# Kernel tuning notes

Measured on AMD Instinct MI355X. Metric: run time of the kernel, lower is better.

## Reference

```python
import jax, jax.numpy as jnp
import numpy as np

B, E, D, M = 128, 8, 512, 4
H = M * D


def setup_inputs() -> dict:
    key = jax.random.key(0)
    k = jax.random.split(key, 6)
    scale1 = 1.0 / np.sqrt(D)
    scale2 = 1.0 / np.sqrt(H)
    return {
        "features": jax.random.normal(k[0], (B, E, D), jnp.float32),
        "target_features": jax.random.normal(k[1], (B, E, D), jnp.float32),
        # batched params for the E x E grid of 2-layer MLPs
        "W1": jax.random.uniform(k[2], (E, E, D, H), jnp.float32, -scale1, scale1),
        "b1": jax.random.uniform(k[3], (E, E, H), jnp.float32, -scale1, scale1),
        "W2": jax.random.uniform(k[4], (E, E, H, D), jnp.float32, -scale2, scale2),
        "b2": jax.random.uniform(k[5], (E, E, D), jnp.float32, -scale2, scale2),
    }


def reference(features, target_features, W1, b1, W2, b2):
    # adapter (a, e) is applied to features[:, a]; all E^2 MLPs batched as grouped GEMMs
    # h: [B, A=E(adapted), E(inner), H]
    h = jax.nn.gelu(jnp.einsum('bad,aedh->baeh', features, W1) + b1, approximate=False)
    out = jnp.einsum('baeh,aehd->baed', h, W2) + b2  # [B, A, E, D]
    # per-(a,e) MSE against target_features[:, a], summed over grid, / num_experts
    err = out - target_features[:, :, None, :]
    per_pair_mse = jnp.mean(err * err, axis=(0, 3))  # [A, E]
    return jnp.sum(per_pair_mse) / E
```

## Files before the change

### kernel.cpp

```cpp
#include <hip/hip_runtime.h>
#include <math.h>


typedef float floatx4 __attribute__((ext_vector_type(4)));
typedef float floatx2 __attribute__((ext_vector_type(2)));
typedef __bf16 bf16x8 __attribute__((ext_vector_type(8)));
typedef unsigned short ushortx8 __attribute__((ext_vector_type(8)));

__device__ __forceinline__ unsigned short f2bf(float f) {
    unsigned u = __builtin_bit_cast(unsigned, f);
    u += 0x7fffu + ((u >> 16) & 1u);
    return (unsigned short)(u >> 16);
}

__device__ __forceinline__ void barrier_nd() {
    asm volatile("s_waitcnt lgkmcnt(0)" ::: "memory");
    __builtin_amdgcn_s_barrier();
}

#define LDSTR 40

__global__ __launch_bounds__(256, 3) void k_gemm1(
    const float* __restrict__ feat, const float* __restrict__ W1,
    const float* __restrict__ b1, unsigned short* __restrict__ hbuf)
{
    __shared__ __align__(16) unsigned short lB[2][128 * LDSTR];

    const int bi = blockIdx.x;
    const int xcd = bi & 7, slot = bi >> 3;
    const int pair = xcd * 8 + (slot >> 4);
    const int nt   = slot & 15;
    const int a    = pair >> 3;
    const int t = threadIdx.x;
    const int w = t >> 6, l = t & 63;
    const int lr = l & 15, lq = l >> 4;
    const int n_base = nt * 128;
    const int m0 = (w & 1) * 64;
    const int n0 = (w >> 1) * 64;

    const float* Bp = W1 + (size_t)pair * 512 * 2048 + n_base + 2 * l;
    const int bk0 = w * 8;
    const float* Af = feat + ((size_t)(m0 + lr) * 8 + a) * 512 + lq * 8;

    floatx2 bpf0[8], bpf1[8];

#define G1_LOADB(KT, S)                                                        \
    {                                                                          \
        _Pragma("unroll")                                                      \
        for (int jj = 0; jj < 8; ++jj)                                         \
            S[jj] = __builtin_nontemporal_load(                                \
                (const floatx2*)(Bp + (size_t)((KT) * 32 + bk0 + jj) * 2048)); \
    }

#define G1_STAGEB(S, BUF)                                                      \
    {                                                                          \
        ushortx8 v0, v1;                                                       \
        _Pragma("unroll")                                                      \
        for (int jj = 0; jj < 8; ++jj) {                                       \
            v0[jj] = f2bf(S[jj][0]);                                           \
            v1[jj] = f2bf(S[jj][1]);                                           \
        }                                                                      \
        *(ushortx8*)&lB[BUF][(2 * l) * LDSTR + bk0] = v0;                      \
        *(ushortx8*)&lB[BUF][(2 * l + 1) * LDSTR + bk0] = v1;                  \
    }

    floatx4 acc[4][4];
    const floatx4 zero = {0.f, 0.f, 0.f, 0.f};
    #pragma unroll
    for (int i = 0; i < 4; ++i)
        #pragma unroll
        for (int j = 0; j < 4; ++j) acc[i][j] = zero;

    G1_LOADB(0, bpf0)
    G1_LOADB(1, bpf1)
    G1_STAGEB(bpf0, 0)
    barrier_nd();

#define G1_BODY(KT, BUF, SLD, SST, GLD, GST)                                   \
    {                                                                          \
        bf16x8 bv[4];                                                          \
        _Pragma("unroll")                                                      \
        for (int j = 0; j < 4; ++j)                                            \
            bv[j] = __builtin_bit_cast(bf16x8,                                 \
                *(const ushortx8*)&lB[BUF][(n0 + 16 * j + lr) * LDSTR + lq * 8]); \
        floatx4 a0[4], a1[4];                                                  \
        _Pragma("unroll")                                                      \
        for (int i = 0; i < 4; ++i) {                                          \
            const float* p = Af + (size_t)(65536 * i) + (KT) * 32;             \
            a0[i] = *(const floatx4*)p;                                        \
            a1[i] = *(const floatx4*)(p + 4);                                  \
        }                                                                      \
        if (GLD) G1_LOADB((KT) + 2, SLD)                                       \
        bf16x8 af[4];                                                          \
        _Pragma("unroll")                                                      \
        for (int i = 0; i < 4; ++i) {                                          \
            ushortx8 v;                                                        \
            _Pragma("unroll")                                                  \
            for (int r = 0; r < 4; ++r) {                                      \
                v[r] = f2bf(a0[i][r]);                                         \
                v[4 + r] = f2bf(a1[i][r]);                                     \
            }                                                                  \
            af[i] = __builtin_bit_cast(bf16x8, v);                             \
        }                                                                      \
        __builtin_amdgcn_s_setprio(1);                                         \
        _Pragma("unroll")                                                      \
        for (int i = 0; i < 4; ++i)                                            \
            _Pragma("unroll")                                                  \
            for (int j = 0; j < 4; ++j)                                        \
                acc[i][j] = __builtin_amdgcn_mfma_f32_16x16x32_bf16(           \
                    af[i], bv[j], acc[i][j], 0, 0, 0);                         \
        __builtin_amdgcn_s_setprio(0);                                         \
        if (GST) G1_STAGEB(SST, (BUF) ^ 1)                                     \
        barrier_nd();                                                          \
    }

    #pragma unroll 1
    for (int kt = 0; kt < 16; kt += 2) {
        G1_BODY(kt,     0, bpf0, bpf1, (kt + 2 < 16), 1)
        G1_BODY(kt + 1, 1, bpf1, bpf0, (kt + 3 < 16), (kt + 2 < 16))
    }

    #pragma unroll
    for (int j = 0; j < 4; ++j) {
        const int col = n_base + n0 + 16 * j + lr;
        const float bias = b1[pair * 2048 + col];
        const size_t cbase = ((size_t)pair * 64 + (col >> 5)) * 128;
        const int cw = col & 31;
        #pragma unroll
        for (int i = 0; i < 4; ++i)
            #pragma unroll
            for (int r = 0; r < 4; ++r) {
                const int row = m0 + 16 * i + lq * 4 + r;
                float x = acc[i][j][r] + bias;
                float g = 0.5f * x * (1.0f + erff(x * 0.70710678118654752f));
                hbuf[(cbase + row) * 32 + cw] = f2bf(g);
            }
    }
#undef G1_LOADB
#undef G1_STAGEB
#undef G1_BODY
}

__global__ __launch_bounds__(256, 2) void k_gemm2(
    const unsigned short* __restrict__ hbuf, const float* __restrict__ W2,
    const float* __restrict__ b2, const float* __restrict__ tgt,
    float* __restrict__ partials)
{
    __shared__ __align__(16) unsigned short lB[2][64 * LDSTR];
    __shared__ float red[4];

    const int bi = blockIdx.x;
    const int xcd = bi & 7, slot = bi >> 3;
    const int pair = xcd * 8 + (slot >> 3);
    const int nt   = slot & 7;
    const int a    = pair >> 3;
    const int t = threadIdx.x;
    const int w = t >> 6, l = t & 63;
    const int lr = l & 15, lq = l >> 4;
    const int n_base = nt * 64;
    const int m0 = (w & 1) * 64;
    const int n0 = (w >> 1) * 32;

    const float* Bp = W2 + (size_t)pair * 2048 * 512 + n_base + l;
    const int bk0 = w * 8;
    const unsigned short* Ahp = hbuf + (size_t)pair * 262144
                              + (size_t)(m0 + lr) * 32 + lq * 8;

    float bpf0[8], bpf1[8];
    ushortx8 apf0[4], apf1[4];

#define G2_LOADB(KT, S)                                                        \
    {                                                                          \
        _Pragma("unroll")                                                      \
        for (int jj = 0; jj < 8; ++jj)                                         \
            S[jj] = __builtin_nontemporal_load(                               \
                Bp + (size_t)((KT) * 32 + bk0 + jj) * 512);                    \
    }

#define G2_LOADA(KT, S)                                                        \
    {                                                                          \
        _Pragma("unroll")                                                      \
        for (int i = 0; i < 4; ++i)                                            \
            S[i] = *(const ushortx8*)(Ahp + (size_t)(KT) * 4096 + i * 512);    \
    }

#define G2_STAGEB(S, BUF)                                                      \
    {                                                                          \
        ushortx8 v;                                                            \
        _Pragma("unroll")                                                      \
        for (int jj = 0; jj < 8; ++jj) v[jj] = f2bf(S[jj]);                    \
        *(ushortx8*)&lB[BUF][l * LDSTR + bk0] = v;                             \
    }

    floatx4 acc[4][2];
    const floatx4 zero = {0.f, 0.f, 0.f, 0.f};
    #pragma unroll
    for (int i = 0; i < 4; ++i)
        #pragma unroll
        for (int j = 0; j < 2; ++j) acc[i][j] = zero;

    G2_LOADB(0, bpf0)
    G2_LOADB(1, bpf1)
    G2_LOADA(0, apf0)
    G2_LOADA(1, apf1)
    G2_STAGEB(bpf0, 0)
    barrier_nd();

#define G2_BODY(KT, BUF, SLD, SST, APF, GLD, GST)                              \
    {                                                                          \
        bf16x8 bv[2];                                                          \
        _Pragma("unroll")                                                      \
        for (int j = 0; j < 2; ++j)                                            \
            bv[j] = __builtin_bit_cast(bf16x8,                                 \
                *(const ushortx8*)&lB[BUF][(n0 + 16 * j + lr) * LDSTR + lq * 8]); \
        if (GLD) G2_LOADB((KT) + 2, SLD)                                       \
        __builtin_amdgcn_s_setprio(1);                                         \
        _Pragma("unroll")                                                      \
        for (int i = 0; i < 4; ++i)                                            \
            _Pragma("unroll")                                                  \
            for (int j = 0; j < 2; ++j)                                        \
                acc[i][j] = __builtin_amdgcn_mfma_f32_16x16x32_bf16(           \
                    __builtin_bit_cast(bf16x8, APF[i]), bv[j],                 \
                    acc[i][j], 0, 0, 0);                                       \
        __builtin_amdgcn_s_setprio(0);                                         \
        if (GLD) G2_LOADA((KT) + 2, APF)                                       \
        if (GST) G2_STAGEB(SST, (BUF) ^ 1)                                     \
        barrier_nd();                                                          \
    }

    #pragma unroll 1
    for (int kt = 0; kt < 64; kt += 2) {
        G2_BODY(kt,     0, bpf0, bpf1, apf0, (kt + 2 < 64), 1)
        G2_BODY(kt + 1, 1, bpf1, bpf0, apf1, (kt + 3 < 64), (kt + 2 < 64))
    }

    float lsum = 0.f;
    #pragma unroll
    for (int j = 0; j < 2; ++j) {
        const int col = n_base + n0 + 16 * j + lr;
        const float bias = b2[pair * 512 + col];
        #pragma unroll
        for (int i = 0; i < 4; ++i)
            #pragma unroll
            for (int r = 0; r < 4; ++r) {
                const int row = m0 + 16 * i + lq * 4 + r;
                float e = acc[i][j][r] + bias - tgt[((size_t)row * 8 + a) * 512 + col];
                lsum += e * e;
            }
    }
    #pragma unroll
    for (int off = 32; off > 0; off >>= 1) lsum += __shfl_down(lsum, off, 64);
    if (l == 0) red[w] = lsum;
    __syncthreads();
    if (t == 0) partials[bi] = red[0] + red[1] + red[2] + red[3];
#undef G2_LOADB
#undef G2_LOADA
#undef G2_STAGEB
#undef G2_BODY
}

__global__ void k_reduce(const float* __restrict__ partials, float* __restrict__ out)
{
    const int t = threadIdx.x;
    float v = partials[t];
    #pragma unroll
    for (int off = 32; off > 0; off >>= 1) v += __shfl_down(v, off, 64);
    __shared__ float red[8];
    if ((t & 63) == 0) red[t >> 6] = v;
    __syncthreads();
    if (t == 0) {
        float s = 0.f;
        #pragma unroll
        for (int i = 0; i < 8; ++i) s += red[i];
        out[0] = s * (1.0f / 524288.0f);
    }
}

extern "C" void kernel_launch(void* const* d_in, const int* in_sizes, int n_in,
                              void* d_out, int out_size, void* d_ws, size_t ws_size,
                              hipStream_t stream) {
    const float* feat = (const float*)d_in[0];
    const float* tgt  = (const float*)d_in[1];
    const float* W1   = (const float*)d_in[2];
    const float* b1   = (const float*)d_in[3];
    const float* W2   = (const float*)d_in[4];
    const float* b2   = (const float*)d_in[5];

    unsigned short* hbuf = (unsigned short*)d_ws;
    float* partials = (float*)((char*)d_ws + (size_t)33554432);
    float* out = (float*)d_out;

    k_gemm1<<<dim3(1024), dim3(256), 0, stream>>>(feat, W1, b1, hbuf);
    k_gemm2<<<dim3(512),  dim3(256), 0, stream>>>(hbuf, W2, b2, tgt, partials);
    k_reduce<<<dim3(1),   dim3(512), 0, stream>>>(partials, out);
}
```

Before: 562.8 us.

## Drop LDS staging; load weights directly into MFMA fragments, pre-convert features to bf16

Both GEMM kernels stop staging the fp32 weight tiles through shared memory with barriers. Each lane now loads the weight elements it needs straight into registers, converts them to bf16 and feeds MFMA, with register double-buffering. A new prep kernel converts the features to bf16 once, and gemm1 uses smaller per-block tiles with twice as many blocks. This removes LDS traffic and barrier stalls. In exchange the weight loads are strided scalar loads (one float per lane per row) instead of vector loads, and the extra launch costs a little.

```diff
diff --git a/kernel.cpp b/kernel.cpp
--- a/kernel.cpp
+++ b/kernel.cpp
@@ -3,9 +3,9 @@
 
 
 typedef float floatx4 __attribute__((ext_vector_type(4)));
-typedef float floatx2 __attribute__((ext_vector_type(2)));
 typedef __bf16 bf16x8 __attribute__((ext_vector_type(8)));
 typedef unsigned short ushortx8 __attribute__((ext_vector_type(8)));
+typedef unsigned short ushortx4 __attribute__((ext_vector_type(4)));
 
 __device__ __forceinline__ unsigned short f2bf(float f) {
     unsigned u = __builtin_bit_cast(unsigned, f);
@@ -13,116 +13,92 @@
     return (unsigned short)(u >> 16);
 }
 
-__device__ __forceinline__ void barrier_nd() {
-    asm volatile("s_waitcnt lgkmcnt(0)" ::: "memory");
-    __builtin_amdgcn_s_barrier();
-}
-
-#define LDSTR 40
+__global__ __launch_bounds__(256) void k_prep(
+    const float* __restrict__ feat, unsigned short* __restrict__ featbf)
+{
+    const int idx = (blockIdx.x * 256 + threadIdx.x) * 4;
+    floatx4 v = *(const floatx4*)(feat + idx);
+    ushortx4 o = { f2bf(v[0]), f2bf(v[1]), f2bf(v[2]), f2bf(v[3]) };
+    *(ushortx4*)(featbf + idx) = o;
+}
 
 __global__ __launch_bounds__(256, 3) void k_gemm1(
-    const float* __restrict__ feat, const float* __restrict__ W1,
+    const unsigned short* __restrict__ featbf, const float* __restrict__ W1,
     const float* __restrict__ b1, unsigned short* __restrict__ hbuf)
 {
-    __shared__ __align__(16) unsigned short lB[2][128 * LDSTR];
-
     const int bi = blockIdx.x;
     const int xcd = bi & 7, slot = bi >> 3;
-    const int pair = xcd * 8 + (slot >> 4);
-    const int nt   = slot & 15;
-    const int a    = pair >> 3;
+    const int pair = xcd * 8 + (slot >> 5);
+    const int nb = slot & 31;
+    const int a = pair >> 3;
     const int t = threadIdx.x;
     const int w = t >> 6, l = t & 63;
     const int lr = l & 15, lq = l >> 4;
-    const int n_base = nt * 128;
-    const int m0 = (w & 1) * 64;
-    const int n0 = (w >> 1) * 64;
-
-    const float* Bp = W1 + (size_t)pair * 512 * 2048 + n_base + 2 * l;
-    const int bk0 = w * 8;
-    const float* Af = feat + ((size_t)(m0 + lr) * 8 + a) * 512 + lq * 8;
-
-    floatx2 bpf0[8], bpf1[8];
-
-#define G1_LOADB(KT, S)                                                        \
-    {                                                                          \
-        _Pragma("unroll")                                                      \
-        for (int jj = 0; jj < 8; ++jj)                                         \
-            S[jj] = __builtin_nontemporal_load(                                \
-                (const floatx2*)(Bp + (size_t)((KT) * 32 + bk0 + jj) * 2048)); \
-    }
-
-#define G1_STAGEB(S, BUF)                                                      \
-    {                                                                          \
-        ushortx8 v0, v1;                                                       \
-        _Pragma("unroll")                                                      \
-        for (int jj = 0; jj < 8; ++jj) {                                       \
-            v0[jj] = f2bf(S[jj][0]);                                           \
-            v1[jj] = f2bf(S[jj][1]);                                           \
-        }                                                                      \
-        *(ushortx8*)&lB[BUF][(2 * l) * LDSTR + bk0] = v0;                      \
-        *(ushortx8*)&lB[BUF][(2 * l + 1) * LDSTR + bk0] = v1;                  \
-    }
-
-    floatx4 acc[4][4];
-    const floatx4 zero = {0.f, 0.f, 0.f, 0.f};
-    #pragma unroll
-    for (int i = 0; i < 4; ++i)
-        #pragma unroll
-        for (int j = 0; j < 4; ++j) acc[i][j] = zero;
-
-    G1_LOADB(0, bpf0)
-    G1_LOADB(1, bpf1)
-    G1_STAGEB(bpf0, 0)
-    barrier_nd();
-
-#define G1_BODY(KT, BUF, SLD, SST, GLD, GST)                                   \
-    {                                                                          \
-        bf16x8 bv[4];                                                          \
-        _Pragma("unroll")                                                      \
-        for (int j = 0; j < 4; ++j)                                            \
-            bv[j] = __builtin_bit_cast(bf16x8,                                 \
-                *(const ushortx8*)&lB[BUF][(n0 + 16 * j + lr) * LDSTR + lq * 8]); \
-        floatx4 a0[4], a1[4];                                                  \
-        _Pragma("unroll")                                                      \
-        for (int i = 0; i < 4; ++i) {                                          \
-            const float* p = Af + (size_t)(65536 * i) + (KT) * 32;             \
-            a0[i] = *(const floatx4*)p;                                        \
-            a1[i] = *(const floatx4*)(p + 4);                                  \
-        }                                                                      \
-        if (GLD) G1_LOADB((KT) + 2, SLD)                                       \
-        bf16x8 af[4];                                                          \
-        _Pragma("unroll")                                                      \
-        for (int i = 0; i < 4; ++i) {                                          \
+    const int mh = w & 1, ns = w >> 1;
+    const int n_base = nb * 64 + ns * 32;
+
+    const float* W1p = W1 + (size_t)pair * (512 * 2048) + n_base + lr;
+    const unsigned short* Ap =
+        featbf + ((size_t)(mh * 64 + lr) * 8 + a) * 512 + lq * 8;
+
+    ushortx8 a0[4], a1[4];
+    float w0[2][8], w1[2][8];
+
+#define LDA1(KT, S)                                                            \
+    {                                                                          \
+        _Pragma("unroll")                                                      \
+        for (int i = 0; i < 4; ++i)                                            \
+            S[i] = *(const ushortx8*)(Ap + (size_t)i * 65536 + (KT) * 32);     \
+    }
+#define LDW1(KT, S)                                                            \
+    {                                                                          \
+        _Pragma("unroll")                                                      \
+        for (int j = 0; j < 2; ++j)                                            \
+            _Pragma("unroll")                                                  \
+            for (int jj = 0; jj < 8; ++jj)                                     \
+                S[j][jj] = __builtin_nontemporal_load(                         \
+                    W1p + 16 * j + (size_t)((KT) * 32 + lq * 8 + jj) * 2048);  \
+    }
+#define CM1(WS, AS)                                                            \
+    {                                                                          \
+        bf16x8 wf[2];                                                          \
+        _Pragma("unroll")                                                      \
+        for (int j = 0; j < 2; ++j) {                                          \
             ushortx8 v;                                                        \
             _Pragma("unroll")                                                  \
-            for (int r = 0; r < 4; ++r) {                                      \
-                v[r] = f2bf(a0[i][r]);                                         \
-                v[4 + r] = f2bf(a1[i][r]);                                     \
-            }                                                                  \
-            af[i] = __builtin_bit_cast(bf16x8, v);                             \
+            for (int e = 0; e < 8; ++e) v[e] = f2bf(WS[j][e]);                 \
+            wf[j] = __builtin_bit_cast(bf16x8, v);                             \
         }                                                                      \
         __builtin_amdgcn_s_setprio(1);                                         \
         _Pragma("unroll")                                                      \
         for (int i = 0; i < 4; ++i)                                            \
             _Pragma("unroll")                                                  \
-            for (int j = 0; j < 4; ++j)                                        \
+            for (int j = 0; j < 2; ++j)                                        \
                 acc[i][j] = __builtin_amdgcn_mfma_f32_16x16x32_bf16(           \
-                    af[i], bv[j], acc[i][j], 0, 0, 0);                         \
+                    __builtin_bit_cast(bf16x8, AS[i]), wf[j], acc[i][j],       \
+                    0, 0, 0);                                                  \
         __builtin_amdgcn_s_setprio(0);                                         \
-        if (GST) G1_STAGEB(SST, (BUF) ^ 1)                                     \
-        barrier_nd();                                                          \
-    }
-
+    }
+
+    floatx4 acc[4][2];
+    const floatx4 zero = {0.f, 0.f, 0.f, 0.f};
+    #pragma unroll
+    for (int i = 0; i < 4; ++i)
+        #pragma unroll
+        for (int j = 0; j < 2; ++j) acc[i][j] = zero;
+
+    LDW1(0, w0) LDA1(0, a0)
     #pragma unroll 1
     for (int kt = 0; kt < 16; kt += 2) {
-        G1_BODY(kt,     0, bpf0, bpf1, (kt + 2 < 16), 1)
-        G1_BODY(kt + 1, 1, bpf1, bpf0, (kt + 3 < 16), (kt + 2 < 16))
-    }
-
-    #pragma unroll
-    for (int j = 0; j < 4; ++j) {
-        const int col = n_base + n0 + 16 * j + lr;
+        LDW1(kt + 1, w1) LDA1(kt + 1, a1)
+        CM1(w0, a0)
+        if (kt + 2 < 16) { LDW1(kt + 2, w0) LDA1(kt + 2, a0) }
+        CM1(w1, a1)
+    }
+
+    #pragma unroll
+    for (int j = 0; j < 2; ++j) {
+        const int col = n_base + 16 * j + lr;
         const float bias = b1[pair * 2048 + col];
         const size_t cbase = ((size_t)pair * 64 + (col >> 5)) * 128;
         const int cw = col & 31;
@@ -130,15 +106,15 @@
         for (int i = 0; i < 4; ++i)
             #pragma unroll
             for (int r = 0; r < 4; ++r) {
-                const int row = m0 + 16 * i + lq * 4 + r;
+                const int row = mh * 64 + 16 * i + lq * 4 + r;
                 float x = acc[i][j][r] + bias;
                 float g = 0.5f * x * (1.0f + erff(x * 0.70710678118654752f));
                 hbuf[(cbase + row) * 32 + cw] = f2bf(g);
             }
     }
-#undef G1_LOADB
-#undef G1_STAGEB
-#undef G1_BODY
+#undef LDA1
+#undef LDW1
+#undef CM1
 }
 
 __global__ __launch_bounds__(256, 2) void k_gemm2(
@@ -146,50 +122,60 @@
     const float* __restrict__ b2, const float* __restrict__ tgt,
     float* __restrict__ partials)
 {
-    __shared__ __align__(16) unsigned short lB[2][64 * LDSTR];
     __shared__ float red[4];
 
     const int bi = blockIdx.x;
     const int xcd = bi & 7, slot = bi >> 3;
     const int pair = xcd * 8 + (slot >> 3);
-    const int nt   = slot & 7;
-    const int a    = pair >> 3;
+    const int nb = slot & 7;
+    const int a = pair >> 3;
     const int t = threadIdx.x;
     const int w = t >> 6, l = t & 63;
     const int lr = l & 15, lq = l >> 4;
-    const int n_base = nt * 64;
-    const int m0 = (w & 1) * 64;
-    const int n0 = (w >> 1) * 32;
-
-    const float* Bp = W2 + (size_t)pair * 2048 * 512 + n_base + l;
-    const int bk0 = w * 8;
-    const unsigned short* Ahp = hbuf + (size_t)pair * 262144
-                              + (size_t)(m0 + lr) * 32 + lq * 8;
-
-    float bpf0[8], bpf1[8];
-    ushortx8 apf0[4], apf1[4];
-
-#define G2_LOADB(KT, S)                                                        \
-    {                                                                          \
-        _Pragma("unroll")                                                      \
-        for (int jj = 0; jj < 8; ++jj)                                         \
-            S[jj] = __builtin_nontemporal_load(                               \
-                Bp + (size_t)((KT) * 32 + bk0 + jj) * 512);                    \
-    }
-
-#define G2_LOADA(KT, S)                                                        \
-    {                                                                          \
-        _Pragma("unroll")                                                      \
-        for (int i = 0; i < 4; ++i)                                            \
-            S[i] = *(const ushortx8*)(Ahp + (size_t)(KT) * 4096 + i * 512);    \
-    }
-
-#define G2_STAGEB(S, BUF)                                                      \
-    {                                                                          \
-        ushortx8 v;                                                            \
-        _Pragma("unroll")                                                      \
-        for (int jj = 0; jj < 8; ++jj) v[jj] = f2bf(S[jj]);                    \
-        *(ushortx8*)&lB[BUF][l * LDSTR + bk0] = v;                             \
+    const int mh = w & 1, ns = w >> 1;
+    const int n_base = nb * 64 + ns * 32;
+
+    const float* W2p = W2 + (size_t)pair * (2048 * 512) + n_base + lr;
+    const unsigned short* Ap = hbuf + (size_t)pair * 262144
+                             + (size_t)(mh * 64 + lr) * 32 + lq * 8;
+
+    ushortx8 a0[4], a1[4];
+    float w0[2][8], w1[2][8];
+
+#define LDA2(KT, S)                                                            \
+    {                                                                          \
+        _Pragma("unroll")                                                      \
+        for (int i = 0; i < 4; ++i)                                            \
+            S[i] = *(const ushortx8*)(Ap + (size_t)(KT) * 4096 + i * 512);     \
+    }
+#define LDW2(KT, S)                                                            \
+    {                                                                          \
+        _Pragma("unroll")                                                      \
+        for (int j = 0; j < 2; ++j)                                            \
+            _Pragma("unroll")                                                  \
+            for (int jj = 0; jj < 8; ++jj)                                     \
+                S[j][jj] = __builtin_nontemporal_load(                         \
+                    W2p + 16 * j + (size_t)((KT) * 32 + lq * 8 + jj) * 512);   \
+    }
+#define CM2(WS, AS)                                                            \
+    {                                                                          \
+        bf16x8 wf[2];                                                          \
+        _Pragma("unroll")                                                      \
+        for (int j = 0; j < 2; ++j) {                                          \
+            ushortx8 v;                                                        \
+            _Pragma("unroll")                                                  \
+            for (int e = 0; e < 8; ++e) v[e] = f2bf(WS[j][e]);                 \
+            wf[j] = __builtin_bit_cast(bf16x8, v);                             \
+        }                                                                      \
+        __builtin_amdgcn_s_setprio(1);                                         \
+        _Pragma("unroll")                                                      \
+        for (int i = 0; i < 4; ++i)                                            \
+            _Pragma("unroll")                                                  \
+            for (int j = 0; j < 2; ++j)                                        \
+                acc[i][j] = __builtin_amdgcn_mfma_f32_16x16x32_bf16(           \
+                    __builtin_bit_cast(bf16x8, AS[i]), wf[j], acc[i][j],       \
+                    0, 0, 0);                                                  \
+        __builtin_amdgcn_s_setprio(0);                                         \
     }
 
     floatx4 acc[4][2];
@@ -199,51 +185,25 @@
         #pragma unroll
         for (int j = 0; j < 2; ++j) acc[i][j] = zero;
 
-    G2_LOADB(0, bpf0)
-    G2_LOADB(1, bpf1)
-    G2_LOADA(0, apf0)
-    G2_LOADA(1, apf1)
-    G2_STAGEB(bpf0, 0)
-    barrier_nd();
-
-#define G2_BODY(KT, BUF, SLD, SST, APF, GLD, GST)                              \
-    {                                                                          \
-        bf16x8 bv[2];                                                          \
-        _Pragma("unroll")                                                      \
-        for (int j = 0; j < 2; ++j)                                            \
-            bv[j] = __builtin_bit_cast(bf16x8,                                 \
-                *(const ushortx8*)&lB[BUF][(n0 + 16 * j + lr) * LDSTR + lq * 8]); \
-        if (GLD) G2_LOADB((KT) + 2, SLD)                                       \
-        __builtin_amdgcn_s_setprio(1);                                         \
-        _Pragma("unroll")                                                      \
-        for (int i = 0; i < 4; ++i)                                            \
-            _Pragma("unroll")                                                  \
-            for (int j = 0; j < 2; ++j)                                        \
-                acc[i][j] = __builtin_amdgcn_mfma_f32_16x16x32_bf16(           \
-                    __builtin_bit_cast(bf16x8, APF[i]), bv[j],                 \
-                    acc[i][j], 0, 0, 0);                                       \
-        __builtin_amdgcn_s_setprio(0);                                         \
-        if (GLD) G2_LOADA((KT) + 2, APF)                                       \
-        if (GST) G2_STAGEB(SST, (BUF) ^ 1)                                     \
-        barrier_nd();                                                          \
-    }
-
+    LDW2(0, w0) LDA2(0, a0)
     #pragma unroll 1
     for (int kt = 0; kt < 64; kt += 2) {
-        G2_BODY(kt,     0, bpf0, bpf1, apf0, (kt + 2 < 64), 1)
-        G2_BODY(kt + 1, 1, bpf1, bpf0, apf1, (kt + 3 < 64), (kt + 2 < 64))
+        LDW2(kt + 1, w1) LDA2(kt + 1, a1)
+        CM2(w0, a0)
+        if (kt + 2 < 64) { LDW2(kt + 2, w0) LDA2(kt + 2, a0) }
+        CM2(w1, a1)
     }
 
     float lsum = 0.f;
     #pragma unroll
     for (int j = 0; j < 2; ++j) {
-        const int col = n_base + n0 + 16 * j + lr;
+        const int col = n_base + 16 * j + lr;
         const float bias = b2[pair * 512 + col];
         #pragma unroll
         for (int i = 0; i < 4; ++i)
             #pragma unroll
             for (int r = 0; r < 4; ++r) {
-                const int row = m0 + 16 * i + lq * 4 + r;
+                const int row = mh * 64 + 16 * i + lq * 4 + r;
                 float e = acc[i][j][r] + bias - tgt[((size_t)row * 8 + a) * 512 + col];
                 lsum += e * e;
             }
@@ -253,10 +213,9 @@
     if (l == 0) red[w] = lsum;
     __syncthreads();
     if (t == 0) partials[bi] = red[0] + red[1] + red[2] + red[3];
-#undef G2_LOADB
-#undef G2_LOADA
-#undef G2_STAGEB
-#undef G2_BODY
+#undef LDA2
+#undef LDW2
+#undef CM2
 }
 
 __global__ void k_reduce(const float* __restrict__ partials, float* __restrict__ out)
@@ -286,11 +245,13 @@
     const float* W2   = (const float*)d_in[4];
     const float* b2   = (const float*)d_in[5];
 
-    unsigned short* hbuf = (unsigned short*)d_ws;
-    float* partials = (float*)((char*)d_ws + (size_t)33554432);
+    unsigned short* hbuf   = (unsigned short*)d_ws;
+    unsigned short* featbf = (unsigned short*)((char*)d_ws + 33554432);
+    float* partials = (float*)((char*)d_ws + 33554432 + 1048576);
     float* out = (float*)d_out;
 
-    k_gemm1<<<dim3(1024), dim3(256), 0, stream>>>(feat, W1, b1, hbuf);
+    k_prep <<<dim3(512),  dim3(256), 0, stream>>>(feat, featbf);
+    k_gemm1<<<dim3(2048), dim3(256), 0, stream>>>(featbf, W1, b1, hbuf);
     k_gemm2<<<dim3(512),  dim3(256), 0, stream>>>(hbuf, W2, b2, tgt, partials);
     k_reduce<<<dim3(1),   dim3(512), 0, stream>>>(partials, out);
 }
```

Result: slower. 695.6 us (+23.6%).
